# Kernel optimization log

Measured on AMD Instinct MI355X. Metric: run time of the kernel, lower is better.

## Reference

```python
import jax, jax.numpy as jnp
import numpy as np

N_NODES = 10000
N_EDGES = 200000
NODE_DIM = 128
EDGE_DIM = 16
CONV_DIM = 64
HEADS = 5
NEG_SLOPE = 0.2


def gatv2_layer(x, src, dst, edge_attr, Wl, bl, We, att, bias):
    # PyG GATv2Conv, share_weights=True, concat=False, add_self_loops=True, eval mode
    N = x.shape[0]
    H, C = att.shape
    xl = (x @ Wl + bl).reshape(N, H, C)  # [N,H,C]; x_r = x_l (share_weights)
    # self loops, edge_attr fill_value='mean' (mean of incoming edge_attr per node)
    deg = jax.ops.segment_sum(jnp.ones(dst.shape[0], x.dtype), dst, num_segments=N)
    loop_attr = jax.ops.segment_sum(edge_attr, dst, num_segments=N) / jnp.maximum(deg, 1.0)[:, None]
    loop = jnp.arange(N, dtype=src.dtype)
    src_f = jnp.concatenate([src, loop])
    dst_f = jnp.concatenate([dst, loop])
    ea = jnp.concatenate([edge_attr, loop_attr], axis=0)
    e_emb = (ea @ We).reshape(-1, H, C)  # [E+N,H,C]
    m = jax.nn.leaky_relu(xl[src_f] + xl[dst_f] + e_emb, NEG_SLOPE)
    score = jnp.einsum('ehc,hc->eh', m, att)  # [E+N,H]
    # per-destination softmax over incoming edges
    smax = jax.ops.segment_max(score, dst_f, num_segments=N)
    ex = jnp.exp(score - smax[dst_f])
    denom = jax.ops.segment_sum(ex, dst_f, num_segments=N)
    alpha = ex / denom[dst_f]
    out = jax.ops.segment_sum(alpha[:, :, None] * xl[src_f], dst_f, num_segments=N)
    return out.mean(axis=1) + bias  # concat=False -> mean over heads


def setup_inputs() -> dict:
    key = jax.random.key(0)
    ks = jax.random.split(key, 32)
    inp = {
        'x': jax.random.normal(ks[0], (N_NODES, NODE_DIM), jnp.float32),
        'edge_index': jax.random.randint(ks[1], (2, N_EDGES), 0, N_NODES, dtype=jnp.int32),
        'edge_attr': jax.random.normal(ks[2], (N_EDGES, EDGE_DIM), jnp.float32),
    }
    in_dims = [NODE_DIM, CONV_DIM, CONV_DIM]
    HC = HEADS * CONV_DIM
    k = 3
    for l in range(3):
        d = in_dims[l]
        inp[f'Wl{l}'] = jax.random.normal(ks[k], (d, HC), jnp.float32) / np.float32(np.sqrt(d)); k += 1
        inp[f'bl{l}'] = jnp.zeros((HC,), jnp.float32)
        inp[f'We{l}'] = jax.random.normal(ks[k], (EDGE_DIM, HC), jnp.float32) / np.float32(np.sqrt(EDGE_DIM)); k += 1
        inp[f'att{l}'] = jax.random.normal(ks[k], (HEADS, CONV_DIM), jnp.float32) / np.float32(np.sqrt(CONV_DIM)); k += 1
        inp[f'b{l}'] = jnp.zeros((CONV_DIM,), jnp.float32)
    return inp


def reference(x, edge_index, edge_attr,
              Wl0, bl0, We0, att0, b0,
              Wl1, bl1, We1, att1, b1,
              Wl2, bl2, We2, att2, b2):
    src, dst = edge_index[0], edge_index[1]
    h = x
    layers = [(Wl0, bl0, We0, att0, b0), (Wl1, bl1, We1, att1, b1), (Wl2, bl2, We2, att2, b2)]
    for Wl, bl, We, att, b in layers:
        h = gatv2_layer(h, src, dst, edge_attr, Wl, bl, We, att, b)
        h = jax.nn.elu(h)
    return h
```

## Files before the change

kernel.cpp:

```cpp
#include <hip/hip_runtime.h>
#include <hip/hip_bf16.h>


#define NN 10000
#define NE 200000
#define ND 128
#define ED 16
#define CD 64
#define NH 5
#define HC 320
#define EF 210000
#define EFP 210048
#define NEG 0.2f
#define SB 103

__global__ void k_count(const int* __restrict__ dst, int* __restrict__ deg) {
  int e = blockIdx.x * blockDim.x + threadIdx.x;
  if (e >= NE) return;
  atomicAdd(&deg[dst[e]], 1);
}

__global__ __launch_bounds__(1024) void k_scan(const int* __restrict__ deg,
                                               int* __restrict__ rowptr) {
  __shared__ int part[1024];
  int t = threadIdx.x;
  int base = t * 10;
  int local[10];
  int s = 0;
  #pragma unroll
  for (int j = 0; j < 10; j++) {
    int i = base + j;
    local[j] = (i < NN) ? deg[i] : 0;
    s += local[j];
  }
  part[t] = s;
  __syncthreads();
  for (int off = 1; off < 1024; off <<= 1) {
    int v = (t >= off) ? part[t - off] : 0;
    __syncthreads();
    part[t] += v;
    __syncthreads();
  }
  int prefix = (t > 0) ? part[t - 1] : 0;
  #pragma unroll
  for (int j = 0; j < 10; j++) {
    int i = base + j;
    if (i < NN) rowptr[i] = prefix;
    prefix += local[j];
  }
  if (t == 1023) rowptr[NN] = prefix;
}

__global__ void k_fill(const int* __restrict__ ei, const int* __restrict__ rowptr,
                       int* __restrict__ cursor, int* __restrict__ csr_eid,
                       int* __restrict__ csr_src, int* __restrict__ csr_dst) {
  int e = blockIdx.x * blockDim.x + threadIdx.x;
  if (e >= NE) return;
  int d = ei[NE + e];
  int slot = atomicAdd(&cursor[d], 1);
  int pos = rowptr[d] + slot;
  csr_eid[pos] = e;
  csr_src[pos] = ei[e];
  csr_dst[pos] = d;
}

__global__ __launch_bounds__(256) void k_loopattr(const int* __restrict__ csr_eid,
                                                  const int* __restrict__ rowptr,
                                                  const float* __restrict__ eattr,
                                                  float* __restrict__ loop_attr) {
  int wave = threadIdx.x >> 6, lane = threadIdx.x & 63;
  int d = blockIdx.x * 4 + wave;
  if (d >= NN) return;
  int g = lane >> 4, k = lane & 15;
  int b = rowptr[d], n = rowptr[d + 1] - b;
  float s = 0.f;
  for (int i = g; i < n; i += 4)
    s += eattr[(size_t)csr_eid[b + i] * ED + k];
  s += __shfl_xor(s, 16, 64);
  s += __shfl_xor(s, 32, 64);
  if (g == 0) loop_attr[d * ED + k] = s / fmaxf((float)n, 1.0f);
}

__global__ void k_eacsr(const int* __restrict__ csr_eid, const float* __restrict__ eattr,
                        float* __restrict__ ea_csr) {
  int idx = blockIdx.x * blockDim.x + threadIdx.x;
  if (idx >= NE * 4) return;
  int p = idx >> 2, q = idx & 3;
  const float4* sp = (const float4*)(eattr + (size_t)csr_eid[p] * ED);
  ((float4*)(ea_csr + (size_t)p * ED))[q] = sp[q];
}

__global__ void k_wet3(const float* __restrict__ We0, const float* __restrict__ We1,
                       const float* __restrict__ We2, float* __restrict__ WeT) {
  int i = blockIdx.x * blockDim.x + threadIdx.x;
  if (i >= 3 * ED * HC) return;
  int l = i / (ED * HC), r = i % (ED * HC);
  int hc = r >> 4, k = r & 15;
  const float* src = (l == 0) ? We0 : (l == 1) ? We1 : We2;
  WeT[i] = src[k * HC + hc];
}

template <int D>
__global__ __launch_bounds__(320) void k_xl(const float* __restrict__ h,
                                            const float* __restrict__ Wl,
                                            const float* __restrict__ bl,
                                            float* __restrict__ xl) {
  constexpr int NPB = 8;
  int node0 = blockIdx.x * NPB;
  int t = threadIdx.x;
  float acc[NPB];
  #pragma unroll
  for (int i = 0; i < NPB; i++) acc[i] = 0.f;
  for (int k = 0; k < D; k += 4) {
    float w0 = Wl[(k + 0) * HC + t];
    float w1 = Wl[(k + 1) * HC + t];
    float w2 = Wl[(k + 2) * HC + t];
    float w3 = Wl[(k + 3) * HC + t];
    #pragma unroll
    for (int i = 0; i < NPB; i++) {
      float4 hv = *(const float4*)(h + (size_t)(node0 + i) * D + k);
      acc[i] += hv.x * w0 + hv.y * w1 + hv.z * w2 + hv.w * w3;
    }
  }
  float bv = bl[t];
  #pragma unroll
  for (int i = 0; i < NPB; i++)
    xl[(size_t)(node0 + i) * HC + t] = acc[i] + bv;
}

__device__ __forceinline__ float dot4(float4 a, float4 b) {
  return a.x * b.x + a.y * b.y + a.z * b.z + a.w * b.w;
}

__global__ __launch_bounds__(256) void k_score(
    const int* __restrict__ csr_src, const int* __restrict__ csr_dst,
    const float* __restrict__ ea_csr, const float* __restrict__ loop_attr,
    const float* __restrict__ xl, const float* __restrict__ WeT,
    const float* __restrict__ att, float* __restrict__ wP) {
  int bid = blockIdx.x;
  int lb = (bid & 7) * SB + (bid >> 3);
  int p = lb * 256 + threadIdx.x;
  if (p >= EF) return;
  int h = blockIdx.y;
  int s, d;
  const float* ea;
  if (p < NE) { s = csr_src[p]; d = csr_dst[p]; ea = ea_csr + (size_t)p * ED; }
  else        { s = d = p - NE; ea = loop_attr + (size_t)(p - NE) * ED; }
  float4 ea4[4];
  {
    const float4* q = (const float4*)ea;
    ea4[0] = q[0]; ea4[1] = q[1]; ea4[2] = q[2]; ea4[3] = q[3];
  }
  const float* xsrow = xl + (size_t)s * HC + h * CD;
  const float* xdrow = xl + (size_t)d * HC + h * CD;
  const float* wrow  = WeT + h * CD * ED;
  const float* arow  = att + h * CD;
  float sc = 0.f;
  #pragma unroll 4
  for (int cb = 0; cb < CD; cb += 4) {
    float4 xs4 = *(const float4*)(xsrow + cb);
    float4 xd4 = *(const float4*)(xdrow + cb);
    const float4* w0 = (const float4*)(wrow + (cb + 0) * ED);
    const float4* w1 = (const float4*)(wrow + (cb + 1) * ED);
    const float4* w2 = (const float4*)(wrow + (cb + 2) * ED);
    const float4* w3 = (const float4*)(wrow + (cb + 3) * ED);
    float z0 = xs4.x + xd4.x + dot4(ea4[0], w0[0]) + dot4(ea4[1], w0[1]) +
               dot4(ea4[2], w0[2]) + dot4(ea4[3], w0[3]);
    float z1 = xs4.y + xd4.y + dot4(ea4[0], w1[0]) + dot4(ea4[1], w1[1]) +
               dot4(ea4[2], w1[2]) + dot4(ea4[3], w1[3]);
    float z2 = xs4.z + xd4.z + dot4(ea4[0], w2[0]) + dot4(ea4[1], w2[1]) +
               dot4(ea4[2], w2[2]) + dot4(ea4[3], w2[3]);
    float z3 = xs4.w + xd4.w + dot4(ea4[0], w3[0]) + dot4(ea4[1], w3[1]) +
               dot4(ea4[2], w3[2]) + dot4(ea4[3], w3[3]);
    z0 *= (z0 > 0.f) ? 1.0f : NEG;
    z1 *= (z1 > 0.f) ? 1.0f : NEG;
    z2 *= (z2 > 0.f) ? 1.0f : NEG;
    z3 *= (z3 > 0.f) ? 1.0f : NEG;
    float4 a4 = *(const float4*)(arow + cb);
    sc += a4.x * z0 + a4.y * z1 + a4.z * z2 + a4.w * z3;
  }
  sc = fminf(fmaxf(sc, -60.f), 60.f);
  wP[(size_t)h * EFP + p] = __expf(sc);
}

template <bool LAST>
__global__ __launch_bounds__(320) void k_aggxl(
    const int* __restrict__ csr_src, const int* __restrict__ rowptr,
    const float* __restrict__ wP, const float* __restrict__ xl_in,
    const float* __restrict__ bias,
    const float* __restrict__ Wl, const float* __restrict__ bl,
    float* __restrict__ outp) {
  __shared__ float s_v[NH][CD];
  __shared__ float s_h[CD];
  int t = threadIdx.x;
  int h = t >> 6, lane = t & 63;
  int d = blockIdx.x;
  int b0 = rowptr[d], n = rowptr[d + 1] - b0;
  const float* sp = wP + (size_t)h * EFP;
  const float* xlh = xl_in + h * CD + lane;
  float dn = sp[NE + d];
  float acc = dn * xlh[(size_t)d * HC];
  int p = b0, pe = b0 + n;
  for (; p + 4 <= pe; p += 4) {
    int s0 = csr_src[p], s1 = csr_src[p + 1], s2 = csr_src[p + 2], s3 = csr_src[p + 3];
    float w0 = sp[p], w1 = sp[p + 1], w2 = sp[p + 2], w3 = sp[p + 3];
    float x0 = xlh[(size_t)s0 * HC];
    float x1 = xlh[(size_t)s1 * HC];
    float x2 = xlh[(size_t)s2 * HC];
    float x3 = xlh[(size_t)s3 * HC];
    dn += (w0 + w1) + (w2 + w3);
    acc += w0 * x0 + w1 * x1 + w2 * x2 + w3 * x3;
  }
  for (; p < pe; p++) {
    int s0 = csr_src[p];
    float w0 = sp[p];
    dn += w0;
    acc += w0 * xlh[(size_t)s0 * HC];
  }
  s_v[h][lane] = acc / dn;
  __syncthreads();
  if (t < CD) {
    float v = s_v[0][t] + s_v[1][t] + s_v[2][t] + s_v[3][t] + s_v[4][t];
    v = v * (1.0f / NH) + bias[t];
    v = v > 0.f ? v : expm1f(v);
    if constexpr (LAST) outp[(size_t)d * CD + t] = v;
    else s_h[t] = v;
  }
  if constexpr (!LAST) {
    __syncthreads();
    float a2 = bl[t];
    #pragma unroll 8
    for (int k = 0; k < CD; k++)
      a2 += s_h[k] * Wl[k * HC + t];
    outp[(size_t)d * HC + t] = a2;
  }
}

extern "C" void kernel_launch(void* const* d_in, const int* in_sizes, int n_in,
                              void* d_out, int out_size, void* d_ws, size_t ws_size,
                              hipStream_t stream) {
  const float* x = (const float*)d_in[0];
  const int* ei = (const int*)d_in[1];
  const float* eattr = (const float*)d_in[2];

  char* w = (char*)d_ws;
  int* degi      = (int*)w;                 w += NN * 4;
  int* cursor    = (int*)w;                 w += NN * 4;
  int* rowptr    = (int*)w;                 w += (NN + 1) * 4;
  int* csr_eid   = (int*)w;                 w += NE * 4;
  int* csr_src   = (int*)w;                 w += NE * 4;
  int* csr_dst   = (int*)w;                 w += NE * 4;
  float* loop_attr = (float*)w;             w += (size_t)NN * ED * 4;
  float* ea_csr  = (float*)w;               w += (size_t)NE * ED * 4;
  float* xlA     = (float*)w;               w += (size_t)NN * HC * 4;
  float* xlB     = (float*)w;               w += (size_t)NN * HC * 4;
  float* wPbuf   = (float*)w;               w += (size_t)NH * EFP * 4;
  float* WeT     = (float*)w;               w += (size_t)3 * ED * HC * 4;

  const float* Wl0  = (const float*)d_in[3];
  const float* bl0  = (const float*)d_in[4];
  const float* att0 = (const float*)d_in[6];
  const float* b0   = (const float*)d_in[7];
  const float* Wl1  = (const float*)d_in[8];
  const float* bl1  = (const float*)d_in[9];
  const float* att1 = (const float*)d_in[11];
  const float* b1   = (const float*)d_in[12];
  const float* Wl2  = (const float*)d_in[13];
  const float* bl2  = (const float*)d_in[14];
  const float* att2 = (const float*)d_in[16];
  const float* b2   = (const float*)d_in[17];

  hipMemsetAsync(degi, 0, NN * 4, stream);
  hipMemsetAsync(cursor, 0, NN * 4, stream);
  k_count<<<(NE + 255) / 256, 256, 0, stream>>>(ei + NE, degi);
  k_scan<<<1, 1024, 0, stream>>>(degi, rowptr);
  k_fill<<<(NE + 255) / 256, 256, 0, stream>>>(ei, rowptr, cursor, csr_eid, csr_src, csr_dst);
  k_loopattr<<<(NN + 3) / 4, 256, 0, stream>>>(csr_eid, rowptr, eattr, loop_attr);
  k_eacsr<<<(NE * 4 + 255) / 256, 256, 0, stream>>>(csr_eid, eattr, ea_csr);
  k_wet3<<<(3 * ED * HC + 255) / 256, 256, 0, stream>>>(
      (const float*)d_in[5], (const float*)d_in[10], (const float*)d_in[15], WeT);

  k_xl<ND><<<NN / 8, 320, 0, stream>>>(x, Wl0, bl0, xlA);

  dim3 gs(8 * SB, NH);
  k_score<<<gs, 256, 0, stream>>>(csr_src, csr_dst, ea_csr, loop_attr,
                                  xlA, WeT, att0, wPbuf);
  k_aggxl<false><<<NN, 320, 0, stream>>>(csr_src, rowptr, wPbuf, xlA, b0,
                                         Wl1, bl1, xlB);
  k_score<<<gs, 256, 0, stream>>>(csr_src, csr_dst, ea_csr, loop_attr,
                                  xlB, WeT + ED * HC, att1, wPbuf);
  k_aggxl<false><<<NN, 320, 0, stream>>>(csr_src, rowptr, wPbuf, xlB, b1,
                                         Wl2, bl2, xlA);
  k_score<<<gs, 256, 0, stream>>>(csr_src, csr_dst, ea_csr, loop_attr,
                                  xlA, WeT + 2 * ED * HC, att2, wPbuf);
  k_aggxl<true><<<NN, 320, 0, stream>>>(csr_src, rowptr, wPbuf, xlA, b2,
                                        nullptr, nullptr, (float*)d_out);
}
```

Baseline: 533.9 us.

## Fuse edge scoring with softmax aggregation per 3-node block, split projection out

Replaces the separate score kernel, which wrote exp-scores to a global buffer, and the aggregation kernel with one fused kernel. Each block handles 3 destination nodes: it computes per-head edge weights into shared memory and then aggregates from there. The next layer's linear projection moves back into the standalone k_xl kernel rather than staying fused into aggregation, and csr_dst is no longer built. The intent is to cut the global traffic and launches for the score buffer. The cost is that score work is now spread across 64 lanes per head per small block, which may underuse lanes. Shared storage caps at MAXP=384 edges per block, so a block with more incoming edges (including self-loops) would compute wrong results.

```diff
diff --git a/kernel.cpp b/kernel.cpp
--- a/kernel.cpp
+++ b/kernel.cpp
@@ -9,10 +9,11 @@
 #define CD 64
 #define NH 5
 #define HC 320
-#define EF 210000
-#define EFP 210048
 #define NEG 0.2f
-#define SB 103
+#define NPB 3
+#define NB 3334
+#define SWZ 417
+#define MAXP 384
 
 __global__ void k_count(const int* __restrict__ dst, int* __restrict__ deg) {
   int e = blockIdx.x * blockDim.x + threadIdx.x;
@@ -53,7 +54,7 @@
 
 __global__ void k_fill(const int* __restrict__ ei, const int* __restrict__ rowptr,
                        int* __restrict__ cursor, int* __restrict__ csr_eid,
-                       int* __restrict__ csr_src, int* __restrict__ csr_dst) {
+                       int* __restrict__ csr_src) {
   int e = blockIdx.x * blockDim.x + threadIdx.x;
   if (e >= NE) return;
   int d = ei[NE + e];
@@ -61,7 +62,6 @@
   int pos = rowptr[d] + slot;
   csr_eid[pos] = e;
   csr_src[pos] = ei[e];
-  csr_dst[pos] = d;
 }
 
 __global__ __launch_bounds__(256) void k_loopattr(const int* __restrict__ csr_eid,
@@ -105,26 +105,26 @@
                                             const float* __restrict__ Wl,
                                             const float* __restrict__ bl,
                                             float* __restrict__ xl) {
-  constexpr int NPB = 8;
-  int node0 = blockIdx.x * NPB;
+  constexpr int NP = 8;
+  int node0 = blockIdx.x * NP;
   int t = threadIdx.x;
-  float acc[NPB];
-  #pragma unroll
-  for (int i = 0; i < NPB; i++) acc[i] = 0.f;
+  float acc[NP];
+  #pragma unroll
+  for (int i = 0; i < NP; i++) acc[i] = 0.f;
   for (int k = 0; k < D; k += 4) {
     float w0 = Wl[(k + 0) * HC + t];
     float w1 = Wl[(k + 1) * HC + t];
     float w2 = Wl[(k + 2) * HC + t];
     float w3 = Wl[(k + 3) * HC + t];
     #pragma unroll
-    for (int i = 0; i < NPB; i++) {
+    for (int i = 0; i < NP; i++) {
       float4 hv = *(const float4*)(h + (size_t)(node0 + i) * D + k);
       acc[i] += hv.x * w0 + hv.y * w1 + hv.z * w2 + hv.w * w3;
     }
   }
   float bv = bl[t];
   #pragma unroll
-  for (int i = 0; i < NPB; i++)
+  for (int i = 0; i < NP; i++)
     xl[(size_t)(node0 + i) * HC + t] = acc[i] + bv;
 }
 
@@ -132,107 +132,118 @@
   return a.x * b.x + a.y * b.y + a.z * b.z + a.w * b.w;
 }
 
-__global__ __launch_bounds__(256) void k_score(
-    const int* __restrict__ csr_src, const int* __restrict__ csr_dst,
+__global__ __launch_bounds__(320) void k_fga(
+    const int* __restrict__ csr_src, const int* __restrict__ rowptr,
     const float* __restrict__ ea_csr, const float* __restrict__ loop_attr,
     const float* __restrict__ xl, const float* __restrict__ WeT,
-    const float* __restrict__ att, float* __restrict__ wP) {
+    const float* __restrict__ att, const float* __restrict__ bias,
+    float* __restrict__ out) {
+  __shared__ float s_w[NH][MAXP];
+  __shared__ float s_v[NH][NPB][CD];
   int bid = blockIdx.x;
-  int lb = (bid & 7) * SB + (bid >> 3);
-  int p = lb * 256 + threadIdx.x;
-  if (p >= EF) return;
-  int h = blockIdx.y;
-  int s, d;
-  const float* ea;
-  if (p < NE) { s = csr_src[p]; d = csr_dst[p]; ea = ea_csr + (size_t)p * ED; }
-  else        { s = d = p - NE; ea = loop_attr + (size_t)(p - NE) * ED; }
-  float4 ea4[4];
-  {
-    const float4* q = (const float4*)ea;
-    ea4[0] = q[0]; ea4[1] = q[1]; ea4[2] = q[2]; ea4[3] = q[3];
-  }
-  const float* xsrow = xl + (size_t)s * HC + h * CD;
-  const float* xdrow = xl + (size_t)d * HC + h * CD;
-  const float* wrow  = WeT + h * CD * ED;
-  const float* arow  = att + h * CD;
-  float sc = 0.f;
-  #pragma unroll 4
-  for (int cb = 0; cb < CD; cb += 4) {
-    float4 xs4 = *(const float4*)(xsrow + cb);
-    float4 xd4 = *(const float4*)(xdrow + cb);
-    const float4* w0 = (const float4*)(wrow + (cb + 0) * ED);
-    const float4* w1 = (const float4*)(wrow + (cb + 1) * ED);
-    const float4* w2 = (const float4*)(wrow + (cb + 2) * ED);
-    const float4* w3 = (const float4*)(wrow + (cb + 3) * ED);
-    float z0 = xs4.x + xd4.x + dot4(ea4[0], w0[0]) + dot4(ea4[1], w0[1]) +
-               dot4(ea4[2], w0[2]) + dot4(ea4[3], w0[3]);
-    float z1 = xs4.y + xd4.y + dot4(ea4[0], w1[0]) + dot4(ea4[1], w1[1]) +
-               dot4(ea4[2], w1[2]) + dot4(ea4[3], w1[3]);
-    float z2 = xs4.z + xd4.z + dot4(ea4[0], w2[0]) + dot4(ea4[1], w2[1]) +
-               dot4(ea4[2], w2[2]) + dot4(ea4[3], w2[3]);
-    float z3 = xs4.w + xd4.w + dot4(ea4[0], w3[0]) + dot4(ea4[1], w3[1]) +
-               dot4(ea4[2], w3[2]) + dot4(ea4[3], w3[3]);
-    z0 *= (z0 > 0.f) ? 1.0f : NEG;
-    z1 *= (z1 > 0.f) ? 1.0f : NEG;
-    z2 *= (z2 > 0.f) ? 1.0f : NEG;
-    z3 *= (z3 > 0.f) ? 1.0f : NEG;
-    float4 a4 = *(const float4*)(arow + cb);
-    sc += a4.x * z0 + a4.y * z1 + a4.z * z2 + a4.w * z3;
-  }
-  sc = fminf(fmaxf(sc, -60.f), 60.f);
-  wP[(size_t)h * EFP + p] = __expf(sc);
-}
-
-template <bool LAST>
-__global__ __launch_bounds__(320) void k_aggxl(
-    const int* __restrict__ csr_src, const int* __restrict__ rowptr,
-    const float* __restrict__ wP, const float* __restrict__ xl_in,
-    const float* __restrict__ bias,
-    const float* __restrict__ Wl, const float* __restrict__ bl,
-    float* __restrict__ outp) {
-  __shared__ float s_v[NH][CD];
-  __shared__ float s_h[CD];
+  int lb = (bid & 7) * SWZ + (bid >> 3);
+  if (lb >= NB) return;
+  int node0 = lb * NPB;
+  int nnodes = min(NPB, NN - node0);
+  int r0 = rowptr[node0];
+  int rEnd = rowptr[node0 + nnodes];
+  int rb1 = (nnodes > 1) ? rowptr[node0 + 1] : rEnd;
+  int rb2 = (nnodes > 2) ? rowptr[node0 + 2] : rEnd;
+  int n_real = rEnd - r0;
+  int ntot = n_real + nnodes;
+
+  int h = threadIdx.x >> 6, lane = threadIdx.x & 63;
+  const float* wrow = WeT + h * CD * ED;
+  const float* arow = att + h * CD;
+
+  for (int pos = lane; pos < ntot; pos += 64) {
+    int s, d;
+    const float* ea;
+    if (pos < n_real) {
+      int p = r0 + pos;
+      s = csr_src[p];
+      d = node0 + (p >= rb1) + (p >= rb2);
+      ea = ea_csr + (size_t)p * ED;
+    } else {
+      int j = pos - n_real;
+      s = d = node0 + j;
+      ea = loop_attr + (size_t)(node0 + j) * ED;
+    }
+    float4 ea4[4];
+    {
+      const float4* q = (const float4*)ea;
+      ea4[0] = q[0]; ea4[1] = q[1]; ea4[2] = q[2]; ea4[3] = q[3];
+    }
+    const float* xsrow = xl + (size_t)s * HC + h * CD;
+    const float* xdrow = xl + (size_t)d * HC + h * CD;
+    float sc = 0.f;
+    #pragma unroll 4
+    for (int cb = 0; cb < CD; cb += 4) {
+      float4 xs4 = *(const float4*)(xsrow + cb);
+      float4 xd4 = *(const float4*)(xdrow + cb);
+      const float4* w0 = (const float4*)(wrow + (cb + 0) * ED);
+      const float4* w1 = (const float4*)(wrow + (cb + 1) * ED);
+      const float4* w2 = (const float4*)(wrow + (cb + 2) * ED);
+      const float4* w3 = (const float4*)(wrow + (cb + 3) * ED);
+      float z0 = xs4.x + xd4.x + dot4(ea4[0], w0[0]) + dot4(ea4[1], w0[1]) +
+                 dot4(ea4[2], w0[2]) + dot4(ea4[3], w0[3]);
+      float z1 = xs4.y + xd4.y + dot4(ea4[0], w1[0]) + dot4(ea4[1], w1[1]) +
+                 dot4(ea4[2], w1[2]) + dot4(ea4[3], w1[3]);
+      float z2 = xs4.z + xd4.z + dot4(ea4[0], w2[0]) + dot4(ea4[1], w2[1]) +
+                 dot4(ea4[2], w2[2]) + dot4(ea4[3], w2[3]);
+      float z3 = xs4.w + xd4.w + dot4(ea4[0], w3[0]) + dot4(ea4[1], w3[1]) +
+                 dot4(ea4[2], w3[2]) + dot4(ea4[3], w3[3]);
+      z0 *= (z0 > 0.f) ? 1.0f : NEG;
+      z1 *= (z1 > 0.f) ? 1.0f : NEG;
+      z2 *= (z2 > 0.f) ? 1.0f : NEG;
+      z3 *= (z3 > 0.f) ? 1.0f : NEG;
+      float4 a4 = *(const float4*)(arow + cb);
+      sc += a4.x * z0 + a4.y * z1 + a4.z * z2 + a4.w * z3;
+    }
+    sc = fminf(fmaxf(sc, -60.f), 60.f);
+    if (pos < MAXP) s_w[h][pos] = __expf(sc);
+  }
+  __syncthreads();
+
+  const float* xlh = xl + h * CD + lane;
+  #pragma unroll
+  for (int j = 0; j < NPB; j++) {
+    if (j >= nnodes) break;
+    int d = node0 + j;
+    int pj0 = ((j == 0) ? r0 : (j == 1) ? rb1 : rb2) - r0;
+    int pj1 = ((j == 0) ? rb1 : (j == 1) ? rb2 : rEnd) - r0;
+    float wS = s_w[h][n_real + j];
+    float dn = wS;
+    float acc = wS * xlh[(size_t)d * HC];
+    int p = pj0;
+    for (; p + 4 <= pj1; p += 4) {
+      int s0 = csr_src[r0 + p], s1 = csr_src[r0 + p + 1];
+      int s2 = csr_src[r0 + p + 2], s3 = csr_src[r0 + p + 3];
+      float w0 = s_w[h][p], w1 = s_w[h][p + 1], w2 = s_w[h][p + 2], w3 = s_w[h][p + 3];
+      float x0 = xlh[(size_t)s0 * HC];
+      float x1 = xlh[(size_t)s1 * HC];
+      float x2 = xlh[(size_t)s2 * HC];
+      float x3 = xlh[(size_t)s3 * HC];
+      dn += (w0 + w1) + (w2 + w3);
+      acc += w0 * x0 + w1 * x1 + w2 * x2 + w3 * x3;
+    }
+    for (; p < pj1; p++) {
+      int s0 = csr_src[r0 + p];
+      float w0 = s_w[h][p];
+      dn += w0;
+      acc += w0 * xlh[(size_t)s0 * HC];
+    }
+    s_v[h][j][lane] = acc / dn;
+  }
+  __syncthreads();
+
   int t = threadIdx.x;
-  int h = t >> 6, lane = t & 63;
-  int d = blockIdx.x;
-  int b0 = rowptr[d], n = rowptr[d + 1] - b0;
-  const float* sp = wP + (size_t)h * EFP;
-  const float* xlh = xl_in + h * CD + lane;
-  float dn = sp[NE + d];
-  float acc = dn * xlh[(size_t)d * HC];
-  int p = b0, pe = b0 + n;
-  for (; p + 4 <= pe; p += 4) {
-    int s0 = csr_src[p], s1 = csr_src[p + 1], s2 = csr_src[p + 2], s3 = csr_src[p + 3];
-    float w0 = sp[p], w1 = sp[p + 1], w2 = sp[p + 2], w3 = sp[p + 3];
-    float x0 = xlh[(size_t)s0 * HC];
-    float x1 = xlh[(size_t)s1 * HC];
-    float x2 = xlh[(size_t)s2 * HC];
-    float x3 = xlh[(size_t)s3 * HC];
-    dn += (w0 + w1) + (w2 + w3);
-    acc += w0 * x0 + w1 * x1 + w2 * x2 + w3 * x3;
-  }
-  for (; p < pe; p++) {
-    int s0 = csr_src[p];
-    float w0 = sp[p];
-    dn += w0;
-    acc += w0 * xlh[(size_t)s0 * HC];
-  }
-  s_v[h][lane] = acc / dn;
-  __syncthreads();
-  if (t < CD) {
-    float v = s_v[0][t] + s_v[1][t] + s_v[2][t] + s_v[3][t] + s_v[4][t];
-    v = v * (1.0f / NH) + bias[t];
+  if (t < nnodes * CD) {
+    int j = t >> 6, c = t & 63;
+    float v = s_v[0][j][c] + s_v[1][j][c] + s_v[2][j][c] + s_v[3][j][c] + s_v[4][j][c];
+    v = v * (1.0f / NH) + bias[c];
     v = v > 0.f ? v : expm1f(v);
-    if constexpr (LAST) outp[(size_t)d * CD + t] = v;
-    else s_h[t] = v;
-  }
-  if constexpr (!LAST) {
-    __syncthreads();
-    float a2 = bl[t];
-    #pragma unroll 8
-    for (int k = 0; k < CD; k++)
-      a2 += s_h[k] * Wl[k * HC + t];
-    outp[(size_t)d * HC + t] = a2;
+    out[(size_t)(node0 + j) * CD + c] = v;
   }
 }
 
@@ -249,12 +260,10 @@
   int* rowptr    = (int*)w;                 w += (NN + 1) * 4;
   int* csr_eid   = (int*)w;                 w += NE * 4;
   int* csr_src   = (int*)w;                 w += NE * 4;
-  int* csr_dst   = (int*)w;                 w += NE * 4;
   float* loop_attr = (float*)w;             w += (size_t)NN * ED * 4;
   float* ea_csr  = (float*)w;               w += (size_t)NE * ED * 4;
   float* xlA     = (float*)w;               w += (size_t)NN * HC * 4;
-  float* xlB     = (float*)w;               w += (size_t)NN * HC * 4;
-  float* wPbuf   = (float*)w;               w += (size_t)NH * EFP * 4;
+  float* hbuf    = (float*)w;               w += (size_t)NN * CD * 4;
   float* WeT     = (float*)w;               w += (size_t)3 * ED * HC * 4;
 
   const float* Wl0  = (const float*)d_in[3];
@@ -274,25 +283,19 @@
   hipMemsetAsync(cursor, 0, NN * 4, stream);
   k_count<<<(NE + 255) / 256, 256, 0, stream>>>(ei + NE, degi);
   k_scan<<<1, 1024, 0, stream>>>(degi, rowptr);
-  k_fill<<<(NE + 255) / 256, 256, 0, stream>>>(ei, rowptr, cursor, csr_eid, csr_src, csr_dst);
+  k_fill<<<(NE + 255) / 256, 256, 0, stream>>>(ei, rowptr, cursor, csr_eid, csr_src);
   k_loopattr<<<(NN + 3) / 4, 256, 0, stream>>>(csr_eid, rowptr, eattr, loop_attr);
   k_eacsr<<<(NE * 4 + 255) / 256, 256, 0, stream>>>(csr_eid, eattr, ea_csr);
   k_wet3<<<(3 * ED * HC + 255) / 256, 256, 0, stream>>>(
       (const float*)d_in[5], (const float*)d_in[10], (const float*)d_in[15], WeT);
 
   k_xl<ND><<<NN / 8, 320, 0, stream>>>(x, Wl0, bl0, xlA);
-
-  dim3 gs(8 * SB, NH);
-  k_score<<<gs, 256, 0, stream>>>(csr_src, csr_dst, ea_csr, loop_attr,
-                                  xlA, WeT, att0, wPbuf);
-  k_aggxl<false><<<NN, 320, 0, stream>>>(csr_src, rowptr, wPbuf, xlA, b0,
-                                         Wl1, bl1, xlB);
-  k_score<<<gs, 256, 0, stream>>>(csr_src, csr_dst, ea_csr, loop_attr,
-                                  xlB, WeT + ED * HC, att1, wPbuf);
-  k_aggxl<false><<<NN, 320, 0, stream>>>(csr_src, rowptr, wPbuf, xlB, b1,
-                                         Wl2, bl2, xlA);
-  k_score<<<gs, 256, 0, stream>>>(csr_src, csr_dst, ea_csr, loop_attr,
-                                  xlA, WeT + 2 * ED * HC, att2, wPbuf);
-  k_aggxl<true><<<NN, 320, 0, stream>>>(csr_src, rowptr, wPbuf, xlA, b2,
-                                        nullptr, nullptr, (float*)d_out);
-}
+  k_fga<<<8 * SWZ, 320, 0, stream>>>(csr_src, rowptr, ea_csr, loop_attr,
+                                     xlA, WeT, att0, b0, hbuf);
+  k_xl<CD><<<NN / 8, 320, 0, stream>>>(hbuf, Wl1, bl1, xlA);
+  k_fga<<<8 * SWZ, 320, 0, stream>>>(csr_src, rowptr, ea_csr, loop_attr,
+                                     xlA, WeT + ED * HC, att1, b1, hbuf);
+  k_xl<CD><<<NN / 8, 320, 0, stream>>>(hbuf, Wl2, bl2, xlA);
+  k_fga<<<8 * SWZ, 320, 0, stream>>>(csr_src, rowptr, ea_csr, loop_attr,
+                                     xlA, WeT + 2 * ED * HC, att2, b2, (float*)d_out);
+}
```

After: 1.182 ms. +121.4%, slower.
